# Kernel optimization log

Measured on AMD Instinct MI355X. Metric: run time of the kernel, lower is better.

Reference implementation:

```python
import jax, jax.numpy as jnp
import numpy as np

FACTOR = 2  # self.factor; anchor='edge', interpolation='linear', bound='dft', extrapolate=False


def _resize_axis_linear_dft(x, axis, osz):
    """Linear resize of one axis with periodic ('dft') boundary, anchor='edge'.

    Out-of-FOV samples (|coord| beyond [-0.5, isz-0.5]) are zeroed
    (extrapolate=False). With edge anchor this mask is always all-True,
    but we keep it for faithfulness.
    """
    isz = x.shape[axis]
    # edge anchor: output voxel centers map to input coords
    c = (jnp.arange(osz, dtype=x.dtype) + 0.5) * (isz / osz) - 0.5
    i0 = jnp.floor(c).astype(jnp.int32)
    w1 = c - i0.astype(x.dtype)          # fractional part
    i0w = jnp.mod(i0, isz)               # dft = circular wrap
    i1w = jnp.mod(i0 + 1, isz)
    x0 = jnp.take(x, i0w, axis=axis)
    x1 = jnp.take(x, i1w, axis=axis)
    # broadcast weights along `axis`
    bshape = [1] * x.ndim
    bshape[axis] = osz
    w1b = w1.reshape(bshape)
    inb = ((c >= -0.5) & (c <= isz - 0.5)).astype(x.dtype).reshape(bshape)
    return (x0 * (1.0 - w1b) + x1 * w1b) * inb


def _resize_flow(flow):
    # flow: (batch, ndim, *inshape)
    ishape = flow.shape[2:]
    oshape = tuple(int(s * FACTOR) for s in ishape)
    out = flow
    for d, osz in enumerate(oshape):
        out = _resize_axis_linear_dft(out, axis=2 + d, osz=osz)
    # anchor 'e': rescale displacement magnitude per channel by osz/isz
    scales = jnp.array([o / i for o, i in zip(oshape, ishape)], dtype=flow.dtype)
    scales = scales.reshape((1, len(ishape)) + (1,) * len(ishape))
    return out * scales


def setup_inputs() -> dict:
    key = jax.random.key(0)
    flow = jax.random.normal(key, (2, 3, 96, 96, 96), dtype=jnp.float32)
    return {"flow": flow}


def reference(flow):
    return _resize_flow(flow)
```

## Files before the change

kernel.cpp:

```cpp
#include <hip/hip_runtime.h>


#define ISZ  96
#define OSZ  192
#define NX4  48
#define NTY  24
#define NTZ  96
#define ZSTR (ISZ * ISZ)

typedef float vf4 __attribute__((ext_vector_type(4)));

struct Q4 { float a, b, c, d; };
struct PL { Q4 r0, r1, r2, r3, r4, r5; };

__device__ __forceinline__ Q4 q_wsum(float wl, const Q4& L, float wh, const Q4& H) {
    Q4 q;
    q.a = fmaf(wl, L.a, wh * H.a);
    q.b = fmaf(wl, L.b, wh * H.b);
    q.c = fmaf(wl, L.c, wh * H.c);
    q.d = fmaf(wl, L.d, wh * H.d);
    return q;
}
__device__ __forceinline__ Q4 q_scale(float w, const Q4& Y) {
    Q4 q; q.a = w * Y.a; q.b = w * Y.b; q.c = w * Y.c; q.d = w * Y.d; return q;
}
__device__ __forceinline__ void q_acc(Q4& O, float w, const Q4& Y) {
    O.a = fmaf(w, Y.a, O.a);
    O.b = fmaf(w, Y.b, O.b);
    O.c = fmaf(w, Y.c, O.c);
    O.d = fmaf(w, Y.d, O.d);
}

__global__ __launch_bounds__(64)
void resize_flow_kernel(const float* __restrict__ in, float* __restrict__ out) {
    unsigned bid = blockIdx.x;
    unsigned wid = (bid & 7u) * (gridDim.x >> 3) + (bid >> 3);
    unsigned t   = wid * 64u + threadIdx.x;

    int x4 = (int)(t % NX4);
    unsigned r = t / NX4;
    int ty = (int)(r % NTY); r /= NTY;
    int k  = (int)(r % NTZ);
    int bc = (int)(r / NTZ);

    int xm = 2 * x4;
    int xa = (x4 == 0)       ? ISZ - 1 : xm - 1;
    int xd = (x4 == NX4 - 1) ? 0       : xm + 2;

    int jy  = 4 * ty;
    int ry0 = (jy == 0) ? ISZ - 1 : jy - 1;
    int ry1 = jy, ry2 = jy + 1, ry3 = jy + 2, ry4 = jy + 3;
    int ry5 = (jy + 4 == ISZ) ? 0 : jy + 4;

    int km = (k == 0)       ? ISZ - 1 : k - 1;
    int kp = (k == ISZ - 1) ? 0       : k + 1;

    const float* base = in + (size_t)bc * (ISZ * ZSTR);

    auto ld = [&](const float* row) -> Q4 {
        float2 m = *reinterpret_cast<const float2*>(row + xm);
        Q4 q; q.a = row[xa]; q.b = m.x; q.c = m.y; q.d = row[xd];
        return q;
    };
    auto load_plane = [&](int p) -> PL {
        const float* pp = base + (size_t)p * ZSTR;
        PL L;
        L.r0 = ld(pp + ry0 * ISZ);
        L.r1 = ld(pp + ry1 * ISZ);
        L.r2 = ld(pp + ry2 * ISZ);
        L.r3 = ld(pp + ry3 * ISZ);
        L.r4 = ld(pp + ry4 * ISZ);
        L.r5 = ld(pp + ry5 * ISZ);
        return L;
    };
    auto yblend = [&](const PL& L, Q4* Y) {
        Y[0] = q_wsum(0.25f, L.r0, 0.75f, L.r1);
        Y[1] = q_wsum(0.75f, L.r1, 0.25f, L.r2);
        Y[2] = q_wsum(0.25f, L.r1, 0.75f, L.r2);
        Y[3] = q_wsum(0.75f, L.r2, 0.25f, L.r3);
        Y[4] = q_wsum(0.25f, L.r2, 0.75f, L.r3);
        Y[5] = q_wsum(0.75f, L.r3, 0.25f, L.r4);
        Y[6] = q_wsum(0.25f, L.r3, 0.75f, L.r4);
        Y[7] = q_wsum(0.75f, L.r4, 0.25f, L.r5);
    };

    int oyb = 8 * ty, ozb = 2 * k;
    auto xstore = [&](const Q4& q, int oz, int dy) {
        vf4 o;
        o.x = fmaf(0.25f, q.a, 0.75f * q.b);
        o.y = fmaf(0.75f, q.b, 0.25f * q.c);
        o.z = fmaf(0.25f, q.b, 0.75f * q.c);
        o.w = fmaf(0.75f, q.c, 0.25f * q.d);
        float* p = out + (((size_t)bc * OSZ + oz) * OSZ + (oyb + dy)) * OSZ + 4 * x4;
        *reinterpret_cast<vf4*>(p) = o;
    };

    Q4 Y[8], A[8];

    PL Lm = load_plane(km);
    PL L0 = load_plane(k);

    yblend(Lm, Y);
#pragma unroll
    for (int i = 0; i < 8; ++i) A[i] = q_scale(0.5f, Y[i]);

    PL Lp = load_plane(kp);

    yblend(L0, Y);
#pragma unroll
    for (int i = 0; i < 8; ++i) q_acc(A[i], 1.5f, Y[i]);
#pragma unroll
    for (int i = 0; i < 8; ++i) xstore(A[i], ozb, i);
#pragma unroll
    for (int i = 0; i < 8; ++i) A[i] = q_scale(1.5f, Y[i]);

    yblend(Lp, Y);
#pragma unroll
    for (int i = 0; i < 8; ++i) q_acc(A[i], 0.5f, Y[i]);
#pragma unroll
    for (int i = 0; i < 8; ++i) xstore(A[i], ozb + 1, i);
}

extern "C" void kernel_launch(void* const* d_in, const int* in_sizes, int n_in,
                              void* d_out, int out_size, void* d_ws, size_t ws_size,
                              hipStream_t stream) {
    const float* in = (const float*)d_in[0];
    float* out = (float*)d_out;

    int total = 6 * NTZ * NTY * NX4;
    int block = 64;
    int grid  = total / block;

    resize_flow_kernel<<<grid, block, 0, stream>>>(in, out);
}
```

Baseline: 34.92 us.

## Retile threads to stream four z-planes with sliding plane reuse

Each thread now handles 2 input y-rows across 4 input z-planes (8 output z-slices) instead of 4 y-rows across one z-plane. Adjacent z-planes are y-blended once and reused by rolling through three plane buffers, so z-halo reloads fall from 3 planes per output pair to 6 planes per 8 outputs. The y-halo overhead rises (4 rows per 2 instead of 6 per 4). Total thread count is halved, which lowers parallelism and adds serial work per thread on a memory-bound kernel.

```diff
diff --git a/kernel.cpp b/kernel.cpp
--- a/kernel.cpp
+++ b/kernel.cpp
@@ -4,14 +4,14 @@
 #define ISZ  96
 #define OSZ  192
 #define NX4  48
-#define NTY  24
-#define NTZ  96
+#define NTY  48
+#define NTZ2 24
 #define ZSTR (ISZ * ISZ)
 
 typedef float vf4 __attribute__((ext_vector_type(4)));
 
 struct Q4 { float a, b, c, d; };
-struct PL { Q4 r0, r1, r2, r3, r4, r5; };
+struct PL { Q4 r0, r1, r2, r3; };
 
 __device__ __forceinline__ Q4 q_wsum(float wl, const Q4& L, float wh, const Q4& H) {
     Q4 q;
@@ -20,15 +20,6 @@
     q.c = fmaf(wl, L.c, wh * H.c);
     q.d = fmaf(wl, L.d, wh * H.d);
     return q;
-}
-__device__ __forceinline__ Q4 q_scale(float w, const Q4& Y) {
-    Q4 q; q.a = w * Y.a; q.b = w * Y.b; q.c = w * Y.c; q.d = w * Y.d; return q;
-}
-__device__ __forceinline__ void q_acc(Q4& O, float w, const Q4& Y) {
-    O.a = fmaf(w, Y.a, O.a);
-    O.b = fmaf(w, Y.b, O.b);
-    O.c = fmaf(w, Y.c, O.c);
-    O.d = fmaf(w, Y.d, O.d);
 }
 
 __global__ __launch_bounds__(64)
@@ -39,21 +30,22 @@
 
     int x4 = (int)(t % NX4);
     unsigned r = t / NX4;
-    int ty = (int)(r % NTY); r /= NTY;
-    int k  = (int)(r % NTZ);
-    int bc = (int)(r / NTZ);
+    int ty  = (int)(r % NTY); r /= NTY;
+    int tz2 = (int)(r % NTZ2);
+    int bc  = (int)(r / NTZ2);
 
     int xm = 2 * x4;
     int xa = (x4 == 0)       ? ISZ - 1 : xm - 1;
     int xd = (x4 == NX4 - 1) ? 0       : xm + 2;
 
-    int jy  = 4 * ty;
+    int jy  = 2 * ty;
     int ry0 = (jy == 0) ? ISZ - 1 : jy - 1;
-    int ry1 = jy, ry2 = jy + 1, ry3 = jy + 2, ry4 = jy + 3;
-    int ry5 = (jy + 4 == ISZ) ? 0 : jy + 4;
+    int ry1 = jy, ry2 = jy + 1;
+    int ry3 = (jy + 2 == ISZ) ? 0 : jy + 2;
 
-    int km = (k == 0)       ? ISZ - 1 : k - 1;
-    int kp = (k == ISZ - 1) ? 0       : k + 1;
+    int K  = 4 * tz2;
+    int pm = (K == 0)        ? ISZ - 1 : K - 1;
+    int pp = (K + 4 == ISZ)  ? 0       : K + 4;
 
     const float* base = in + (size_t)bc * (ISZ * ZSTR);
 
@@ -63,14 +55,12 @@
         return q;
     };
     auto load_plane = [&](int p) -> PL {
-        const float* pp = base + (size_t)p * ZSTR;
+        const float* pp_ = base + (size_t)p * ZSTR;
         PL L;
-        L.r0 = ld(pp + ry0 * ISZ);
-        L.r1 = ld(pp + ry1 * ISZ);
-        L.r2 = ld(pp + ry2 * ISZ);
-        L.r3 = ld(pp + ry3 * ISZ);
-        L.r4 = ld(pp + ry4 * ISZ);
-        L.r5 = ld(pp + ry5 * ISZ);
+        L.r0 = ld(pp_ + ry0 * ISZ);
+        L.r1 = ld(pp_ + ry1 * ISZ);
+        L.r2 = ld(pp_ + ry2 * ISZ);
+        L.r3 = ld(pp_ + ry3 * ISZ);
         return L;
     };
     auto yblend = [&](const PL& L, Q4* Y) {
@@ -78,47 +68,51 @@
         Y[1] = q_wsum(0.75f, L.r1, 0.25f, L.r2);
         Y[2] = q_wsum(0.25f, L.r1, 0.75f, L.r2);
         Y[3] = q_wsum(0.75f, L.r2, 0.25f, L.r3);
-        Y[4] = q_wsum(0.25f, L.r2, 0.75f, L.r3);
-        Y[5] = q_wsum(0.75f, L.r3, 0.25f, L.r4);
-        Y[6] = q_wsum(0.25f, L.r3, 0.75f, L.r4);
-        Y[7] = q_wsum(0.75f, L.r4, 0.25f, L.r5);
     };
 
-    int oyb = 8 * ty, ozb = 2 * k;
-    auto xstore = [&](const Q4& q, int oz, int dy) {
-        vf4 o;
-        o.x = fmaf(0.25f, q.a, 0.75f * q.b);
-        o.y = fmaf(0.75f, q.b, 0.25f * q.c);
-        o.z = fmaf(0.25f, q.b, 0.75f * q.c);
-        o.w = fmaf(0.75f, q.c, 0.25f * q.d);
-        float* p = out + (((size_t)bc * OSZ + oz) * OSZ + (oyb + dy)) * OSZ + 4 * x4;
-        *reinterpret_cast<vf4*>(p) = o;
+    int oyb = 4 * ty;
+    auto store4 = [&](float wl, const Q4* YL, float wh, const Q4* YH, int oz) {
+        float* pz = out + (((size_t)bc * OSZ + oz) * OSZ + oyb) * OSZ + 4 * x4;
+#pragma unroll
+        for (int i = 0; i < 4; ++i) {
+            Q4 q = q_wsum(wl, YL[i], wh, YH[i]);
+            vf4 o;
+            o.x = fmaf(0.25f, q.a, 0.75f * q.b);
+            o.y = fmaf(0.75f, q.b, 0.25f * q.c);
+            o.z = fmaf(0.25f, q.b, 0.75f * q.c);
+            o.w = fmaf(0.75f, q.c, 0.25f * q.d);
+            *reinterpret_cast<vf4*>(pz + (size_t)i * OSZ) = o;
+        }
     };
 
-    Q4 Y[8], A[8];
+    Q4 Ya[4], Yb[4], Yc[4];
+    int ozb = 8 * tz2;
 
-    PL Lm = load_plane(km);
-    PL L0 = load_plane(k);
+    PL La = load_plane(pm);
+    PL Lb = load_plane(K);
+    PL Lc = load_plane(K + 1);
 
-    yblend(Lm, Y);
-#pragma unroll
-    for (int i = 0; i < 8; ++i) A[i] = q_scale(0.5f, Y[i]);
+    yblend(La, Ya);
+    yblend(Lb, Yb);
+    La = load_plane(K + 2);
+    store4(0.5f, Ya, 1.5f, Yb, ozb + 0);
 
-    PL Lp = load_plane(kp);
+    yblend(Lc, Yc);
+    store4(1.5f, Yb, 0.5f, Yc, ozb + 1);
+    store4(0.5f, Yb, 1.5f, Yc, ozb + 2);
+    Lb = load_plane(K + 3);
 
-    yblend(L0, Y);
-#pragma unroll
-    for (int i = 0; i < 8; ++i) q_acc(A[i], 1.5f, Y[i]);
-#pragma unroll
-    for (int i = 0; i < 8; ++i) xstore(A[i], ozb, i);
-#pragma unroll
-    for (int i = 0; i < 8; ++i) A[i] = q_scale(1.5f, Y[i]);
+    yblend(La, Ya);
+    store4(1.5f, Yc, 0.5f, Ya, ozb + 3);
+    store4(0.5f, Yc, 1.5f, Ya, ozb + 4);
+    Lc = load_plane(pp);
 
-    yblend(Lp, Y);
-#pragma unroll
-    for (int i = 0; i < 8; ++i) q_acc(A[i], 0.5f, Y[i]);
-#pragma unroll
-    for (int i = 0; i < 8; ++i) xstore(A[i], ozb + 1, i);
+    yblend(Lb, Yb);
+    store4(1.5f, Ya, 0.5f, Yb, ozb + 5);
+    store4(0.5f, Ya, 1.5f, Yb, ozb + 6);
+
+    yblend(Lc, Yc);
+    store4(1.5f, Yb, 0.5f, Yc, ozb + 7);
 }
 
 extern "C" void kernel_launch(void* const* d_in, const int* in_sizes, int n_in,
@@ -127,7 +121,7 @@
     const float* in = (const float*)d_in[0];
     float* out = (float*)d_out;
 
-    int total = 6 * NTZ * NTY * NX4;
+    int total = 6 * NTZ2 * NTY * NX4;
     int block = 64;
     int grid  = total / block;
 
```

After: 36.09 us. 3.4% more time.
